# Performance work log

Measured on AMD Instinct MI355X. Metric: run time of the kernel, lower is better.

The kernel has to match this reference:

```python
import jax, jax.numpy as jnp
import numpy as np

B, S, H = 2, 2048, 2048
NH, HD = 16, 128
TS = 512
RATE = 0.1          # custom_active_rate (used as the sampled mean, deterministic)
ALPHA = 0.5         # ts_ema_alpha
EPS = 1e-6
BASE = 10000.0
K_IDX = int((1.0 - RATE) * TS)   # torch.kthvalue k (1-indexed k-th smallest) = 460


def _rmsnorm(x, w):
    xf = x.astype(jnp.float32)
    var = jnp.mean(xf * xf, axis=-1, keepdims=True)
    return (xf * jax.lax.rsqrt(var + EPS)).astype(x.dtype) * w


def _rope_tables():
    inv = 1.0 / (BASE ** (np.arange(0, HD, 2, dtype=np.float32) / HD))
    t = np.arange(S, dtype=np.float32)
    freqs = np.outer(t, inv)                       # [S, HD/2]
    emb = np.concatenate([freqs, freqs], axis=-1)  # [S, HD]
    return jnp.asarray(np.cos(emb)), jnp.asarray(np.sin(emb))


def _rotate_half(x):
    x1, x2 = jnp.split(x, 2, axis=-1)
    return jnp.concatenate([-x2, x1], axis=-1)


def setup_inputs() -> dict:
    key = jax.random.key(0)
    ks = jax.random.split(key, 9)
    sc = 0.02
    return {
        'hidden_states': jax.random.normal(ks[0], (B, S, H), jnp.float32),
        'last_layer_ts_embedding': jax.random.normal(ks[1], (B, S, TS), jnp.float32),
        'Wq': jax.random.normal(ks[2], (H, H), jnp.float32) * sc,
        'Wk': jax.random.normal(ks[3], (H, H), jnp.float32) * sc,
        'Wv': jax.random.normal(ks[4], (H, H), jnp.float32) * sc,
        'Wo': jax.random.normal(ks[5], (H, H), jnp.float32) * sc,
        'Wts': jax.random.normal(ks[6], (H, TS), jnp.float32) * sc,
        'ts_norm_w': jnp.ones((TS,), jnp.float32),
        'Worig': jax.random.normal(ks[7], (TS, 3 * H), jnp.float32) * sc,
    }


def reference(hidden_states, last_layer_ts_embedding, Wq, Wk, Wv, Wo, Wts, ts_norm_w, Worig):
    # --- custom TS gating path ---
    ts = hidden_states @ Wts                                  # [B,S,TS]
    ts = (1.0 - ALPHA) * ts + ALPHA * last_layer_ts_embedding # EMA with previous layer
    ts = _rmsnorm(ts, ts_norm_w)
    # torch.kthvalue: k-th smallest along last dim, keepdim
    kth = jnp.sort(ts, axis=-1)[..., K_IDX - 1:K_IDX]          # [B,S,1]
    ts_filtered = jax.nn.relu(ts - kth)
    origin = ts_filtered @ Worig                               # [B,S,3H]
    q_add = origin[..., :H]
    k_add = origin[..., H:2 * H]
    v_add = k_add                                              # 'qkv' mode: v uses split[1]

    # --- qkv projections (llama linear, no bias) ---
    q = hidden_states @ Wq + q_add
    k = hidden_states @ Wk + k_add
    v = hidden_states @ Wv + v_add
    q = q.reshape(B, S, NH, HD).transpose(0, 2, 1, 3)          # [B,NH,S,HD]
    k = k.reshape(B, S, NH, HD).transpose(0, 2, 1, 3)
    v = v.reshape(B, S, NH, HD).transpose(0, 2, 1, 3)

    # --- rotary embedding ---
    cos, sin = _rope_tables()                                  # [S,HD]
    cos = cos[None, None]; sin = sin[None, None]
    q = q * cos + _rotate_half(q) * sin
    k = k * cos + _rotate_half(k) * sin

    # --- eager attention: QK^T, causal mask add, fp32 softmax, PV ---
    scores = jnp.einsum('bhqd,bhkd->bhqk', q, k) / jnp.sqrt(jnp.float32(HD))
    causal = jnp.tril(jnp.ones((S, S), bool))
    mask = jnp.where(causal, 0.0, -1e9).astype(scores.dtype)[None, None]
    probs = jax.nn.softmax((scores + mask).astype(jnp.float32), axis=-1).astype(q.dtype)
    attn = jnp.einsum('bhqk,bhkd->bhqd', probs, v)
    attn = attn.transpose(0, 2, 1, 3).reshape(B, S, H)
    return attn @ Wo
```

## Files before the change

kernel.cpp:

```cpp
#include <hip/hip_runtime.h>
#include <cstdint>

typedef __bf16 bf16_t;
typedef __bf16 bf16x8 __attribute__((ext_vector_type(8)));
typedef __bf16 bf16x4 __attribute__((ext_vector_type(4)));
typedef float  f32x4  __attribute__((ext_vector_type(4)));
typedef bf16x8 __attribute__((may_alias)) bf16x8a;
typedef bf16x4 __attribute__((may_alias)) bf16x4a;
typedef f32x4  __attribute__((may_alias)) f32x4a;

#define S_LEN 2048
#define HDIM  2048
#define NHEAD 16
#define HD    128
#define TSD   512
#define BROWS 4096
#define KIDX  459
#define KCAT  2560

__device__ __forceinline__ f32x4 mfma_bf16(bf16x8 a, bf16x8 b, f32x4 c) {
  return __builtin_amdgcn_mfma_f32_16x16x32_bf16(a, b, c, 0, 0, 0);
}

__device__ __forceinline__ void gld_lds16(const bf16_t* g, bf16_t* l) {
  __builtin_amdgcn_global_load_lds(
      (__attribute__((address_space(1))) void*)(void*)const_cast<bf16_t*>(g),
      (__attribute__((address_space(3))) void*)(void*)(l), 16, 0, 0);
}

__device__ __forceinline__ uint32_t pk2(float a, float b) {
  union { bf16_t h; uint16_t u; } ua, ub;
  ua.h = (bf16_t)a; ub.h = (bf16_t)b;
  return (uint32_t)ua.u | ((uint32_t)ub.u << 16);
}

__global__ void k_cvt(const float* __restrict__ in, bf16_t* __restrict__ out, int n) {
  int i = (blockIdx.x * 256 + threadIdx.x) * 4;
  if (i >= n) return;
  f32x4 v = *(const f32x4a*)(in + i);
  bf16x4 o = { (bf16_t)v.x, (bf16_t)v.y, (bf16_t)v.z, (bf16_t)v.w };
  *(bf16x4a*)(out + i) = o;
}

__global__ void k_transpose(const float* __restrict__ in, bf16_t* __restrict__ out,
                            int ldin, int ldout, int koff) {
  __shared__ float tile[32][33];
  int c0 = blockIdx.x * 32, r0 = blockIdx.y * 32;
  int tx = threadIdx.x, ty = threadIdx.y;
  for (int i = ty; i < 32; i += 8)
    tile[i][tx] = in[(size_t)(r0 + i) * ldin + c0 + tx];
  __syncthreads();
  for (int i = ty; i < 32; i += 8)
    out[(size_t)(c0 + i) * ldout + koff + r0 + tx] = (bf16_t)tile[tx][i];
}

__global__ void k_vtrans(const bf16_t* __restrict__ in, bf16_t* __restrict__ out) {
  __shared__ bf16_t t[64][72];
  int s0 = blockIdx.x * 64, d0 = blockIdx.y * 64, bh = blockIdx.z;
  const bf16_t* src = in + (size_t)bh * S_LEN * HD;
  bf16_t* dst = out + (size_t)bh * HD * S_LEN;
  int tid = threadIdx.x;
  for (int g = tid; g < 512; g += 256) {
    int r = g >> 3, cc = g & 7;
    *(bf16x8a*)&t[r][cc * 8] = *(const bf16x8a*)(src + (size_t)(s0 + r) * HD + d0 + cc * 8);
  }
  __syncthreads();
  for (int g = tid; g < 512; g += 256) {
    int dr = g >> 3, sc = g & 7;
    bf16x8 v;
#pragma unroll
    for (int j = 0; j < 8; j++) v[j] = t[sc * 8 + j][dr];
    *(bf16x8a*)(dst + (size_t)(d0 + dr) * S_LEN + s0 + sc * 8) = v;
  }
}

__global__ __launch_bounds__(256)
void k_gemm(const bf16_t* __restrict__ A, const bf16_t* __restrict__ Bt,
            float* __restrict__ outF, int M, int N, int K)
{
  __shared__ __align__(16) bf16_t As[128 * 32];
  __shared__ __align__(16) bf16_t Bs[128 * 32];
  const int tid  = threadIdx.x;
  const int lane = tid & 63, w = tid >> 6;
  const int quad = lane >> 4, l15 = lane & 15;
  const int m0 = blockIdx.y * 128, n0 = blockIdx.x * 128;
  const int wm = (w >> 1) * 64, wn = (w & 1) * 64;

  f32x4 acc[4][4];
#pragma unroll
  for (int i = 0; i < 4; i++)
#pragma unroll
    for (int j = 0; j < 4; j++) { f32x4 z = {0.f,0.f,0.f,0.f}; acc[i][j] = z; }

  const int srow = w * 16 + (lane >> 2);
  const int scol = (lane & 3) * 8;

  for (int k0 = 0; k0 < K; k0 += 32) {
    __syncthreads();
    gld_lds16(A  + (size_t)(m0 +      srow) * K + k0 + scol, As + (size_t)w * 512);
    gld_lds16(A  + (size_t)(m0 + 64 + srow) * K + k0 + scol, As + (size_t)(4 + w) * 512);
    gld_lds16(Bt + (size_t)(n0 +      srow) * K + k0 + scol, Bs + (size_t)w * 512);
    gld_lds16(Bt + (size_t)(n0 + 64 + srow) * K + k0 + scol, Bs + (size_t)(4 + w) * 512);
    __syncthreads();
    bf16x8 af[4], bv[4];
#pragma unroll
    for (int i = 0; i < 4; i++)
      af[i] = *(const bf16x8a*)&As[(wm + i * 16 + l15) * 32 + quad * 8];
#pragma unroll
    for (int j = 0; j < 4; j++)
      bv[j] = *(const bf16x8a*)&Bs[(wn + j * 16 + l15) * 32 + quad * 8];
#pragma unroll
    for (int i = 0; i < 4; i++)
#pragma unroll
      for (int j = 0; j < 4; j++)
        acc[i][j] = mfma_bf16(af[i], bv[j], acc[i][j]);
  }

#pragma unroll
  for (int i = 0; i < 4; i++)
#pragma unroll
    for (int j = 0; j < 4; j++)
#pragma unroll
      for (int r = 0; r < 4; r++) {
        int row = m0 + wm + i * 16 + quad * 4 + r;
        int col = n0 + wn + j * 16 + l15;
        outF[(size_t)row * N + col] = acc[i][j][r];
      }
}

__global__ __launch_bounds__(256)
void k_gemm_qkv(const bf16_t* __restrict__ hsB, const bf16_t* __restrict__ tsf,
                const bf16_t* __restrict__ wcat, bf16_t* __restrict__ outQKV,
                const float* __restrict__ tabC, const float* __restrict__ tabS)
{
  __shared__ __align__(16) bf16_t As[128 * 32];
  __shared__ __align__(16) bf16_t Bs[128 * 32];
  const int tid  = threadIdx.x;
  const int lane = tid & 63, w = tid >> 6;
  const int quad = lane >> 4, l15 = lane & 15;
  const int wi = blockIdx.x >> 4;
  const int n0 = (blockIdx.x & 15) * 128;
  const int m0 = blockIdx.y * 128;
  const int wm = (w >> 1) * 64;
  const bf16_t* Bt = wcat + (size_t)wi * HDIM * KCAT;
  bf16_t* outp = outQKV + (size_t)wi * 8388608;

  int col2[4];
#pragma unroll
  for (int j = 0; j < 4; j++)
    col2[j] = (w & 1) * 32 + (j & 1) * 16 + (j >> 1) * 64 + l15;

  f32x4 acc[4][4];
#pragma unroll
  for (int i = 0; i < 4; i++)
#pragma unroll
    for (int j = 0; j < 4; j++) { f32x4 z = {0.f,0.f,0.f,0.f}; acc[i][j] = z; }

  const int srow = w * 16 + (lane >> 2);
  const int scol = (lane & 3) * 8;

  for (int k0 = 0; k0 < KCAT; k0 += 32) {
    const bf16_t* Ab; int lda, kc;
    if (k0 < HDIM) { Ab = hsB; lda = HDIM; kc = k0; }
    else           { Ab = tsf; lda = TSD;  kc = k0 - HDIM; }
    __syncthreads();
    gld_lds16(Ab + (size_t)(m0 +      srow) * lda + kc + scol, As + (size_t)w * 512);
    gld_lds16(Ab + (size_t)(m0 + 64 + srow) * lda + kc + scol, As + (size_t)(4 + w) * 512);
    gld_lds16(Bt + (size_t)(n0 +      srow) * KCAT + k0 + scol, Bs + (size_t)w * 512);
    gld_lds16(Bt + (size_t)(n0 + 64 + srow) * KCAT + k0 + scol, Bs + (size_t)(4 + w) * 512);
    __syncthreads();
    bf16x8 af[4], bv[4];
#pragma unroll
    for (int i = 0; i < 4; i++)
      af[i] = *(const bf16x8a*)&As[(wm + i * 16 + l15) * 32 + quad * 8];
#pragma unroll
    for (int j = 0; j < 4; j++)
      bv[j] = *(const bf16x8a*)&Bs[col2[j] * 32 + quad * 8];
#pragma unroll
    for (int i = 0; i < 4; i++)
#pragma unroll
      for (int j = 0; j < 4; j++)
        acc[i][j] = mfma_bf16(af[i], bv[j], acc[i][j]);
  }

  const int h = n0 >> 7;
  if (wi == 2) {
#pragma unroll
    for (int i = 0; i < 4; i++)
#pragma unroll
      for (int r = 0; r < 4; r++) {
        int row = m0 + wm + i * 16 + quad * 4 + r;
        int s = row & (S_LEN - 1), b = row >> 11;
        size_t obase = (((size_t)(b * NHEAD + h) * S_LEN) + s) * HD;
#pragma unroll
        for (int j = 0; j < 4; j++)
          outp[obase + col2[j]] = (bf16_t)acc[i][j][r];
      }
  } else {
#pragma unroll
    for (int i = 0; i < 4; i++)
#pragma unroll
      for (int r = 0; r < 4; r++) {
        int row = m0 + wm + i * 16 + quad * 4 + r;
        int s = row & (S_LEN - 1), b = row >> 11;
        size_t obase = (((size_t)(b * NHEAD + h) * S_LEN) + s) * HD;
#pragma unroll
        for (int j = 0; j < 2; j++) {
          int d = (w & 1) * 32 + j * 16 + l15;
          float lo = acc[i][j][r];
          float hi = acc[i][j + 2][r];
          float c  = tabC[s * 64 + d];
          float sn = tabS[s * 64 + d];
          outp[obase + d]      = (bf16_t)(lo * c - hi * sn);
          outp[obase + d + 64] = (bf16_t)(hi * c + lo * sn);
        }
      }
  }
}

__global__ __launch_bounds__(256)
void k_tsproc(const float* __restrict__ ts, const float* __restrict__ lte,
              const float* __restrict__ wn, bf16_t* __restrict__ tsf)
{
  __shared__ float sv[TSD];
  __shared__ float red[4];
  int row = blockIdx.x;
  int t = threadIdx.x;
  const float* tr = ts  + (size_t)row * TSD;
  const float* lr = lte + (size_t)row * TSD;
  float v0 = 0.5f * tr[t] + 0.5f * lr[t];
  float v1 = 0.5f * tr[t + 256] + 0.5f * lr[t + 256];
  float ss = v0 * v0 + v1 * v1;
#pragma unroll
  for (int o = 32; o > 0; o >>= 1) ss += __shfl_down(ss, o);
  int lane = t & 63, wv = t >> 6;
  if (lane == 0) red[wv] = ss;
  __syncthreads();
  float tot = red[0] + red[1] + red[2] + red[3];
  float scl = rsqrtf(tot * (1.0f / TSD) + 1e-6f);
  float n0 = v0 * scl * wn[t];
  float n1 = v1 * scl * wn[t + 256];
  sv[t] = n0; sv[t + 256] = n1;
  __syncthreads();
  for (int k = 2; k <= TSD; k <<= 1) {
    for (int j = k >> 1; j > 0; j >>= 1) {
#pragma unroll
      for (int u = 0; u < 2; u++) {
        int idx = t + u * 256;
        int ixj = idx ^ j;
        if (ixj > idx) {
          float a = sv[idx], b = sv[ixj];
          bool up = ((idx & k) == 0);
          if ((a > b) == up) { sv[idx] = b; sv[ixj] = a; }
        }
      }
      __syncthreads();
    }
  }
  float kth = sv[KIDX];
  tsf[(size_t)row * TSD + t]       = (bf16_t)fmaxf(n0 - kth, 0.0f);
  tsf[(size_t)row * TSD + t + 256] = (bf16_t)fmaxf(n1 - kth, 0.0f);
}

__global__ void k_ropetab(float* __restrict__ tabC, float* __restrict__ tabS) {
  int gid = blockIdx.x * 256 + threadIdx.x;
  int d = gid & 63, s = gid >> 6;
  float inv = powf(10000.0f, (float)(-2 * d) * (1.0f / 128.0f));
  float sn, c;
  sincosf((float)s * inv, &sn, &c);
  tabC[gid] = c; tabS[gid] = sn;
}

__global__ __launch_bounds__(256, 4)
void k_attn(const bf16_t* __restrict__ qb, const bf16_t* __restrict__ kb,
            const bf16_t* __restrict__ vtb, bf16_t* __restrict__ attnB)
{
  __shared__ __align__(16) bf16_t Kt[64 * 128];
  __shared__ __align__(16) bf16_t Vt[128 * 64];

  const int bid = blockIdx.x;
  const int bh  = (bid & 7) + 8 * (bid >> 8);
  static const int qmap[32] = {31,0,30,1,29,2,28,3,27,4,26,5,25,6,24,7,
                               23,8,22,9,21,10,20,11,19,12,18,13,17,14,16,15};
  const int q0 = qmap[((bid >> 3) + (bid >> 8)) & 31] * 64;

  const int tid = threadIdx.x;
  const int lane = tid & 63, w = tid >> 6;
  const int quad = lane >> 4, l15 = lane & 15;

  const bf16_t* Q  = qb  + (size_t)bh * S_LEN * HD;
  const bf16_t* Kg = kb  + (size_t)bh * S_LEN * HD;
  const bf16_t* Vg = vtb + (size_t)bh * HD * S_LEN;

  bf16x8 qf[4];
  {
    const bf16_t* qrow = Q + (size_t)(q0 + w * 16 + l15) * HD;
#pragma unroll
    for (int c = 0; c < 4; c++)
      qf[c] = *(const bf16x8a*)(qrow + c * 32 + quad * 8);
  }

  int kfo[4];
#pragma unroll
  for (int c = 0; c < 4; c++)
    kfo[c] = l15 * 128 + (((c * 4 + quad) ^ (l15 & 7)) * 8);
  int vfo[2];
#pragma unroll
  for (int kc = 0; kc < 2; kc++)
    vfo[kc] = l15 * 64 + (((kc * 4 + quad) ^ (l15 & 7)) * 8);

  int kSrc[4], vSrc[4];
#pragma unroll
  for (int j = 0; j < 4; j++) {
    int G  = (w * 4 + j) * 64 + lane;
    int r  = G >> 4, gl = G & 15;
    kSrc[j] = r * HD + ((gl ^ (r & 7)) * 8);
    int d  = G >> 3, vg = G & 7;
    vSrc[j] = d * S_LEN + ((vg ^ (d & 7)) * 8);
  }

  const int addrA = 4 * (l15 + 32 * (quad & 1));
  const int addrB = addrA + 64;
  const bool selHi = (quad >> 1) != 0;

  f32x4 o[8];
#pragma unroll
  for (int t8 = 0; t8 < 8; t8++) { f32x4 z = {0.f,0.f,0.f,0.f}; o[t8] = z; }
  float m_i = -1e30f, l_i = 0.0f;

  const float scale = 0.08838834764831845f;
  const int kEnd = q0;
  const int qrow_i = q0 + w * 16 + l15;

  for (int k0 = 0; k0 <= kEnd; k0 += 64) {
    {
      const bf16_t* Kgk = Kg + (size_t)k0 * HD;
      const bf16_t* Vgk = Vg + k0;
#pragma unroll
      for (int j = 0; j < 4; j++)
        gld_lds16(Kgk + kSrc[j], Kt + (w * 4 + j) * 512);
#pragma unroll
      for (int j = 0; j < 4; j++)
        gld_lds16(Vgk + vSrc[j], Vt + (w * 4 + j) * 512);
    }
    __syncthreads();

    f32x4 st_[4];
#pragma unroll
    for (int nt = 0; nt < 4; nt++) { f32x4 z = {0.f,0.f,0.f,0.f}; st_[nt] = z; }
    __builtin_amdgcn_s_setprio(1);
#pragma unroll
    for (int nt = 0; nt < 4; nt++)
#pragma unroll
      for (int c = 0; c < 4; c++) {
        bf16x8 kf = *(const bf16x8a*)(Kt + kfo[c] + nt * 2048);
        st_[nt] = mfma_bf16(kf, qf[c], st_[nt]);
      }
    __builtin_amdgcn_s_setprio(0);

    if (k0 == q0) {
#pragma unroll
      for (int nt = 0; nt < 4; nt++)
#pragma unroll
        for (int r = 0; r < 4; r++) {
          int key = k0 + nt * 16 + quad * 4 + r;
          float v = st_[nt][r] * scale;
          st_[nt][r] = (key > qrow_i) ? -1e9f : v;
        }
    } else {
#pragma unroll
      for (int nt = 0; nt < 4; nt++)
#pragma unroll
        for (int r = 0; r < 4; r++)
          st_[nt][r] *= scale;
    }

    float mx = st_[0][0];
#pragma unroll
    for (int nt = 0; nt < 4; nt++)
#pragma unroll
      for (int r = 0; r < 4; r++) mx = fmaxf(mx, st_[nt][r]);
    mx = fmaxf(mx, __shfl_xor(mx, 16));
    mx = fmaxf(mx, __shfl_xor(mx, 32));

    if (__ballot(mx > m_i + 8.0f)) {
      float mnew = fmaxf(m_i, mx);
      float alpha = __expf(m_i - mnew);
      m_i = mnew;
      l_i *= alpha;
#pragma unroll
      for (int t8 = 0; t8 < 8; t8++)
#pragma unroll
        for (int r = 0; r < 4; r++)
          o[t8][r] *= alpha;
    }

    float rs = 0.0f;
#pragma unroll
    for (int nt = 0; nt < 4; nt++)
#pragma unroll
      for (int r = 0; r < 4; r++) {
        float pv = __expf(st_[nt][r] - m_i);
        st_[nt][r] = pv;
        rs += pv;
      }
    rs += __shfl_xor(rs, 16);
    rs += __shfl_xor(rs, 32);
    l_i += rs;

    uint32_t pk[4][2];
#pragma unroll
    for (int nt = 0; nt < 4; nt++) {
      pk[nt][0] = pk2(st_[nt][0], st_[nt][1]);
      pk[nt][1] = pk2(st_[nt][2], st_[nt][3]);
    }

#pragma unroll
    for (int kc = 0; kc < 2; kc++) {
      uint32_t a0 = __builtin_amdgcn_ds_bpermute(addrA, (int)pk[2*kc][0]);
      uint32_t a1 = __builtin_amdgcn_ds_bpermute(addrA, (int)pk[2*kc][1]);
      uint32_t a2 = __builtin_amdgcn_ds_bpermute(addrB, (int)pk[2*kc][0]);
      uint32_t a3 = __builtin_amdgcn_ds_bpermute(addrB, (int)pk[2*kc][1]);
      uint32_t b0 = __builtin_amdgcn_ds_bpermute(addrA, (int)pk[2*kc+1][0]);
      uint32_t b1 = __builtin_amdgcn_ds_bpermute(addrA, (int)pk[2*kc+1][1]);
      uint32_t b2 = __builtin_amdgcn_ds_bpermute(addrB, (int)pk[2*kc+1][0]);
      uint32_t b3 = __builtin_amdgcn_ds_bpermute(addrB, (int)pk[2*kc+1][1]);
      union { bf16x8 v; uint32_t d[4]; } pf;
      pf.d[0] = selHi ? b0 : a0;
      pf.d[1] = selHi ? b1 : a1;
      pf.d[2] = selHi ? b2 : a2;
      pf.d[3] = selHi ? b3 : a3;
      __builtin_amdgcn_s_setprio(1);
#pragma unroll
      for (int t8 = 0; t8 < 8; t8++) {
        bf16x8 vf = *(const bf16x8a*)(Vt + vfo[kc] + t8 * 1024);
        o[t8] = mfma_bf16(vf, pf.v, o[t8]);
      }
      __builtin_amdgcn_s_setprio(0);
    }

    __syncthreads();
  }

  const int b = bh >> 4, h = bh & 15;
  const float rl = 1.0f / l_i;
  uint32_t* outp = (uint32_t*)(attnB + (size_t)(b * S_LEN + qrow_i) * HDIM + h * HD);
#pragma unroll
  for (int t8 = 0; t8 < 8; t8++)
#pragma unroll
    for (int pr = 0; pr < 2; pr++) {
      uint32_t v = pk2(o[t8][2*pr] * rl, o[t8][2*pr+1] * rl);
      outp[t8 * 8 + quad * 2 + pr] = v;
    }
}

extern "C" void kernel_launch(void* const* d_in, const int* in_sizes, int n_in,
                              void* d_out, int out_size, void* d_ws, size_t ws_size,
                              hipStream_t stream) {
  const float* hs    = (const float*)d_in[0];
  const float* lte   = (const float*)d_in[1];
  const float* Wq    = (const float*)d_in[2];
  const float* Wk    = (const float*)d_in[3];
  const float* Wv    = (const float*)d_in[4];
  const float* Wo    = (const float*)d_in[5];
  const float* Wts   = (const float*)d_in[6];
  const float* tsw   = (const float*)d_in[7];
  const float* Worig = (const float*)d_in[8];
  float* out = (float*)d_out;

  char* p = (char*)d_ws;
  bf16_t* hsB   = (bf16_t*)(p);
  bf16_t* wT    = (bf16_t*)(p + 16777216);
  float*  tsB   = (float*)(p + 25165824);
  bf16_t* tsf   = (bf16_t*)(p + 33554432);
  bf16_t* wcat  = (bf16_t*)(p + 37748736);
  bf16_t* attnB = (bf16_t*)(p + 37748736);
  bf16_t* vtb   = (bf16_t*)(p + 54525952);
  bf16_t* qbuf  = (bf16_t*)(p + 71303168);
  bf16_t* kbuf  = (bf16_t*)(p + 88080384);
  bf16_t* vbuf  = (bf16_t*)(p + 104857600);
  float*  tabC  = tsB;
  float*  tabS  = tsB + 131072;
  bf16_t* wcatQ = wcat;
  bf16_t* wcatK = wcat + (size_t)HDIM * KCAT;
  bf16_t* wcatV = wcat + (size_t)2 * HDIM * KCAT;

  k_cvt<<<8192, 256, 0, stream>>>(hs, hsB, BROWS * HDIM);
  k_transpose<<<dim3(16, 64), dim3(32, 8), 0, stream>>>(Wts, wT, 512, 2048, 0);
  k_gemm<<<dim3(4, 32), 256, 0, stream>>>(hsB, wT, tsB, 4096, 512, 2048);
  k_tsproc<<<4096, 256, 0, stream>>>(tsB, lte, tsw, tsf);
  k_ropetab<<<512, 256, 0, stream>>>(tabC, tabS);
  k_transpose<<<dim3(64, 64), dim3(32, 8), 0, stream>>>(Wq, wcatQ, 2048, KCAT, 0);
  k_transpose<<<dim3(64, 16), dim3(32, 8), 0, stream>>>(Worig, wcatQ, 6144, KCAT, 2048);
  k_transpose<<<dim3(64, 64), dim3(32, 8), 0, stream>>>(Wk, wcatK, 2048, KCAT, 0);
  k_transpose<<<dim3(64, 16), dim3(32, 8), 0, stream>>>(Worig + 2048, wcatK, 6144, KCAT, 2048);
  k_transpose<<<dim3(64, 64), dim3(32, 8), 0, stream>>>(Wv, wcatV, 2048, KCAT, 0);
  k_transpose<<<dim3(64, 16), dim3(32, 8), 0, stream>>>(Worig + 2048, wcatV, 6144, KCAT, 2048);
  k_gemm_qkv<<<dim3(48, 32), 256, 0, stream>>>(hsB, tsf, wcat, qbuf, tabC, tabS);
  k_vtrans<<<dim3(32, 2, 32), 256, 0, stream>>>(vbuf, vtb);
  k_transpose<<<dim3(64, 64), dim3(32, 8), 0, stream>>>(Wo, wT, 2048, 2048, 0);
  k_attn<<<1024, 256, 0, stream>>>(qbuf, kbuf, vtb, attnB);
  k_gemm<<<dim3(16, 32), 256, 0, stream>>>(attnB, wT, out, 4096, 2048, 2048);
}
```

Baseline: 603.5 us.

## Double-buffer GEMM LDS tiles with XOR swizzle and grouped block remap

Both GEMM kernels now keep two LDS buffers per operand and prefetch the next K-tile with global_load_lds while the current tile feeds the MFMAs. Synchronisation uses explicit vmcnt/lgkmcnt waits and raw s_barrier calls. The kernels also XOR-swizzle the LDS column groups to cut bank conflicts, raise wave priority around the MFMA block, and remap block indices so neighbouring workgroups are spread across groups for better cache locality. The cost is twice the LDS per block, which may lower occupancy, and the hand-written waitcnt logic is fragile if the compiler reorders loads.

```diff
diff --git a/kernel.cpp b/kernel.cpp
--- a/kernel.cpp
+++ b/kernel.cpp
@@ -17,6 +17,10 @@
 #define BROWS 4096
 #define KIDX  459
 #define KCAT  2560
+
+#define WAITVM4()   asm volatile("s_waitcnt vmcnt(4)" ::: "memory")
+#define WAITVM0()   asm volatile("s_waitcnt vmcnt(0)" ::: "memory")
+#define WAITLGKM0() asm volatile("s_waitcnt lgkmcnt(0)" ::: "memory")
 
 __device__ __forceinline__ f32x4 mfma_bf16(bf16x8 a, bf16x8 b, f32x4 c) {
   return __builtin_amdgcn_mfma_f32_16x16x32_bf16(a, b, c, 0, 0, 0);
@@ -74,46 +78,81 @@
   }
 }
 
+
 __global__ __launch_bounds__(256)
 void k_gemm(const bf16_t* __restrict__ A, const bf16_t* __restrict__ Bt,
             float* __restrict__ outF, int M, int N, int K)
 {
-  __shared__ __align__(16) bf16_t As[128 * 32];
-  __shared__ __align__(16) bf16_t Bs[128 * 32];
+  __shared__ __align__(16) bf16_t As[2][4096];
+  __shared__ __align__(16) bf16_t Bs[2][4096];
+  const int nwg  = gridDim.x * gridDim.y;
+  const int flat = blockIdx.y * gridDim.x + blockIdx.x;
+  const int l    = (flat & 7) * (nwg >> 3) + (flat >> 3);
+  const int bx   = l % gridDim.x, by = l / gridDim.x;
   const int tid  = threadIdx.x;
   const int lane = tid & 63, w = tid >> 6;
   const int quad = lane >> 4, l15 = lane & 15;
-  const int m0 = blockIdx.y * 128, n0 = blockIdx.x * 128;
+  const int m0 = by * 128, n0 = bx * 128;
   const int wm = (w >> 1) * 64, wn = (w & 1) * 64;
 
+  size_t aoff[2], boff[2];
+#pragma unroll
+  for (int j = 0; j < 2; j++) {
+    int G = (w * 2 + j) * 64 + lane;
+    int row = G >> 2, c = G & 3;
+    int cg = c ^ (row & 3);
+    aoff[j] = (size_t)(m0 + row) * K + cg * 8;
+    boff[j] = (size_t)(n0 + row) * K + cg * 8;
+  }
+  const int rg = (quad ^ (l15 & 3)) * 8;
+
   f32x4 acc[4][4];
 #pragma unroll
   for (int i = 0; i < 4; i++)
 #pragma unroll
     for (int j = 0; j < 4; j++) { f32x4 z = {0.f,0.f,0.f,0.f}; acc[i][j] = z; }
 
-  const int srow = w * 16 + (lane >> 2);
-  const int scol = (lane & 3) * 8;
-
-  for (int k0 = 0; k0 < K; k0 += 32) {
-    __syncthreads();
-    gld_lds16(A  + (size_t)(m0 +      srow) * K + k0 + scol, As + (size_t)w * 512);
-    gld_lds16(A  + (size_t)(m0 + 64 + srow) * K + k0 + scol, As + (size_t)(4 + w) * 512);
-    gld_lds16(Bt + (size_t)(n0 +      srow) * K + k0 + scol, Bs + (size_t)w * 512);
-    gld_lds16(Bt + (size_t)(n0 + 64 + srow) * K + k0 + scol, Bs + (size_t)(4 + w) * 512);
-    __syncthreads();
+  const int nt = K >> 5;
+#pragma unroll
+  for (int j = 0; j < 2; j++) {
+    gld_lds16(A  + aoff[j], &As[0][(w * 2 + j) * 512]);
+    gld_lds16(Bt + boff[j], &Bs[0][(w * 2 + j) * 512]);
+  }
+
+  for (int t = 0; t < nt; ++t) {
+    const int cur = t & 1;
+    if (t + 1 < nt) {
+      const int k = (t + 1) * 32;
+#pragma unroll
+      for (int j = 0; j < 2; j++) {
+        gld_lds16(A  + aoff[j] + k, &As[cur ^ 1][(w * 2 + j) * 512]);
+        gld_lds16(Bt + boff[j] + k, &Bs[cur ^ 1][(w * 2 + j) * 512]);
+      }
+      WAITVM4();
+    } else {
+      WAITVM0();
+    }
+    __builtin_amdgcn_s_barrier();
+    __builtin_amdgcn_sched_barrier(0);
+
     bf16x8 af[4], bv[4];
 #pragma unroll
     for (int i = 0; i < 4; i++)
-      af[i] = *(const bf16x8a*)&As[(wm + i * 16 + l15) * 32 + quad * 8];
+      af[i] = *(const bf16x8a*)&As[cur][(wm + i * 16 + l15) * 32 + rg];
 #pragma unroll
     for (int j = 0; j < 4; j++)
-      bv[j] = *(const bf16x8a*)&Bs[(wn + j * 16 + l15) * 32 + quad * 8];
+      bv[j] = *(const bf16x8a*)&Bs[cur][(wn + j * 16 + l15) * 32 + rg];
+    __builtin_amdgcn_s_setprio(1);
 #pragma unroll
     for (int i = 0; i < 4; i++)
 #pragma unroll
       for (int j = 0; j < 4; j++)
         acc[i][j] = mfma_bf16(af[i], bv[j], acc[i][j]);
+    __builtin_amdgcn_s_setprio(0);
+
+    WAITLGKM0();
+    __builtin_amdgcn_s_barrier();
+    __builtin_amdgcn_sched_barrier(0);
   }
 
 #pragma unroll
@@ -133,18 +172,34 @@
                 const bf16_t* __restrict__ wcat, bf16_t* __restrict__ outQKV,
                 const float* __restrict__ tabC, const float* __restrict__ tabS)
 {
-  __shared__ __align__(16) bf16_t As[128 * 32];
-  __shared__ __align__(16) bf16_t Bs[128 * 32];
+  __shared__ __align__(16) bf16_t As[2][4096];
+  __shared__ __align__(16) bf16_t Bs[2][4096];
+  const int nwg  = gridDim.x * gridDim.y;
+  const int flat = blockIdx.y * gridDim.x + blockIdx.x;
+  const int l    = (flat & 7) * (nwg >> 3) + (flat >> 3);
+  const int bx   = l % gridDim.x, by = l / gridDim.x;
   const int tid  = threadIdx.x;
   const int lane = tid & 63, w = tid >> 6;
   const int quad = lane >> 4, l15 = lane & 15;
-  const int wi = blockIdx.x >> 4;
-  const int n0 = (blockIdx.x & 15) * 128;
-  const int m0 = blockIdx.y * 128;
+  const int wi = bx >> 4;
+  const int n0 = (bx & 15) * 128;
+  const int m0 = by * 128;
   const int wm = (w >> 1) * 64;
   const bf16_t* Bt = wcat + (size_t)wi * HDIM * KCAT;
   bf16_t* outp = outQKV + (size_t)wi * 8388608;
 
+  size_t aoffh[2], aofft[2], boff[2];
+#pragma unroll
+  for (int j = 0; j < 2; j++) {
+    int G = (w * 2 + j) * 64 + lane;
+    int row = G >> 2, c = G & 3;
+    int cg = c ^ (row & 3);
+    aoffh[j] = (size_t)(m0 + row) * HDIM + cg * 8;
+    aofft[j] = (size_t)(m0 + row) * TSD  + cg * 8;
+    boff[j]  = (size_t)(n0 + row) * KCAT + cg * 8;
+  }
+  const int rg = (quad ^ (l15 & 3)) * 8;
+
   int col2[4];
 #pragma unroll
   for (int j = 0; j < 4; j++)
@@ -156,31 +211,51 @@
 #pragma unroll
     for (int j = 0; j < 4; j++) { f32x4 z = {0.f,0.f,0.f,0.f}; acc[i][j] = z; }
 
-  const int srow = w * 16 + (lane >> 2);
-  const int scol = (lane & 3) * 8;
-
-  for (int k0 = 0; k0 < KCAT; k0 += 32) {
-    const bf16_t* Ab; int lda, kc;
-    if (k0 < HDIM) { Ab = hsB; lda = HDIM; kc = k0; }
-    else           { Ab = tsf; lda = TSD;  kc = k0 - HDIM; }
-    __syncthreads();
-    gld_lds16(Ab + (size_t)(m0 +      srow) * lda + kc + scol, As + (size_t)w * 512);
-    gld_lds16(Ab + (size_t)(m0 + 64 + srow) * lda + kc + scol, As + (size_t)(4 + w) * 512);
-    gld_lds16(Bt + (size_t)(n0 +      srow) * KCAT + k0 + scol, Bs + (size_t)w * 512);
-    gld_lds16(Bt + (size_t)(n0 + 64 + srow) * KCAT + k0 + scol, Bs + (size_t)(4 + w) * 512);
-    __syncthreads();
+  const int nt = KCAT >> 5;
+#pragma unroll
+  for (int j = 0; j < 2; j++) {
+    gld_lds16(hsB + aoffh[j], &As[0][(w * 2 + j) * 512]);
+    gld_lds16(Bt  + boff[j],  &Bs[0][(w * 2 + j) * 512]);
+  }
+
+  for (int t = 0; t < nt; ++t) {
+    const int cur = t & 1;
+    if (t + 1 < nt) {
+      const int k = (t + 1) * 32;
+#pragma unroll
+      for (int j = 0; j < 2; j++) {
+        const bf16_t* asrc = (k < HDIM) ? (hsB + aoffh[j] + k)
+                                        : (tsf + aofft[j] + (k - HDIM));
+        gld_lds16(asrc, &As[cur ^ 1][(w * 2 + j) * 512]);
+      }
+#pragma unroll
+      for (int j = 0; j < 2; j++)
+        gld_lds16(Bt + boff[j] + k, &Bs[cur ^ 1][(w * 2 + j) * 512]);
+      WAITVM4();
+    } else {
+      WAITVM0();
+    }
+    __builtin_amdgcn_s_barrier();
+    __builtin_amdgcn_sched_barrier(0);
+
     bf16x8 af[4], bv[4];
 #pragma unroll
     for (int i = 0; i < 4; i++)
-      af[i] = *(const bf16x8a*)&As[(wm + i * 16 + l15) * 32 + quad * 8];
+      af[i] = *(const bf16x8a*)&As[cur][(wm + i * 16 + l15) * 32 + rg];
 #pragma unroll
     for (int j = 0; j < 4; j++)
-      bv[j] = *(const bf16x8a*)&Bs[col2[j] * 32 + quad * 8];
+      bv[j] = *(const bf16x8a*)&Bs[cur][col2[j] * 32 + rg];
+    __builtin_amdgcn_s_setprio(1);
 #pragma unroll
     for (int i = 0; i < 4; i++)
 #pragma unroll
       for (int j = 0; j < 4; j++)
         acc[i][j] = mfma_bf16(af[i], bv[j], acc[i][j]);
+    __builtin_amdgcn_s_setprio(0);
+
+    WAITLGKM0();
+    __builtin_amdgcn_s_barrier();
+    __builtin_amdgcn_sched_barrier(0);
   }
 
   const int h = n0 >> 7;
```

New measurement: 612.0 us. Within noise of the previous version (+1.4%).
